# Kernel optimization log

Measured on AMD Instinct MI355X. Metric: run time of the kernel, lower is better.

## Reference

```python
import jax, jax.numpy as jnp
import numpy as np

EMBED_DIM = 1024
NUM_HEADS = 16
HEAD_DIM = EMBED_DIM // NUM_HEADS


def setup_inputs() -> dict:
    key = jax.random.key(0)
    ks = jax.random.split(key, 6)
    s = 1.0 / np.sqrt(EMBED_DIM)
    x = jax.random.normal(ks[0], (2, 2048, EMBED_DIM), dtype=jnp.float32)
    Wk = jax.random.uniform(ks[1], (EMBED_DIM, EMBED_DIM), jnp.float32, -s, s)
    Wq = jax.random.uniform(ks[2], (EMBED_DIM, EMBED_DIM), jnp.float32, -s, s)
    Wv = jax.random.uniform(ks[3], (EMBED_DIM, EMBED_DIM), jnp.float32, -s, s)
    Wo = jax.random.uniform(ks[4], (EMBED_DIM, EMBED_DIM), jnp.float32, -s, s)
    bo = jax.random.uniform(ks[5], (EMBED_DIM,), jnp.float32, -s, s)
    return {"x": x, "Wq": Wq, "Wk": Wk, "Wv": Wv, "Wo": Wo, "bo": bo}


def reference(x, Wq, Wk, Wv, Wo, bo):
    b, s, e = x.shape
    h, d = NUM_HEADS, HEAD_DIM
    scale = d ** (-0.5)
    # nn.Linear: y = x @ W.T ; here W stored as [out, in] -> use W.T
    q = (x @ Wq.T).reshape(b, s, h, d).transpose(0, 2, 1, 3)  # b h s d
    k = (x @ Wk.T).reshape(b, s, h, d).transpose(0, 2, 1, 3)
    v = (x @ Wv.T).reshape(b, s, h, d).transpose(0, 2, 1, 3)
    logits = jnp.einsum('bhqd,bhkd->bhqk', q, k) * scale
    attn = jax.nn.softmax(logits, axis=-1)
    out = jnp.einsum('bhqk,bhkd->bhqd', attn, v)
    out = out.transpose(0, 2, 1, 3).reshape(b, s, e)
    return out @ Wo.T + bo
```

## Files before the change

kernel.cpp:

```cpp
#include <hip/hip_runtime.h>
#include <hip/hip_bf16.h>

using short8 = __attribute__((ext_vector_type(8))) short;
using f32x4  = __attribute__((ext_vector_type(4))) float;
using uint4v = __attribute__((ext_vector_type(4))) unsigned;

#if __has_builtin(__builtin_amdgcn_exp2f)
#define EXP2(x) __builtin_amdgcn_exp2f(x)
#else
#define EXP2(x) exp2f(x)
#endif

#define SOFT_BARRIER()                                            \
    do {                                                          \
        asm volatile("s_waitcnt lgkmcnt(0)" ::: "memory");        \
        __builtin_amdgcn_s_barrier();                             \
    } while (0)

#define VM_BARRIER()                                              \
    do {                                                          \
        asm volatile("s_waitcnt vmcnt(0)" ::: "memory");          \
        __builtin_amdgcn_s_barrier();                             \
    } while (0)

__device__ __forceinline__ short f2bf(float f) {
    union { float f; unsigned u; } v; v.f = f;
    unsigned r = v.u + 0x7fffu + ((v.u >> 16) & 1u);
    return (short)(r >> 16);
}
__device__ __forceinline__ unsigned pack_trunc(float a, float b) {
    union { float f; unsigned u; } ua, ub; ua.f = a; ub.f = b;
#if __has_builtin(__builtin_amdgcn_perm)
    return __builtin_amdgcn_perm(ub.u, ua.u, 0x07060302u);
#else
    return (ub.u & 0xFFFF0000u) | (ua.u >> 16);
#endif
}
__device__ __forceinline__ void async_copy16(const short* g, short* s) {
    __builtin_amdgcn_global_load_lds(
        (const __attribute__((address_space(1))) void*)g,
        (__attribute__((address_space(3))) void*)s, 16, 0, 0);
}

__global__ __launch_bounds__(256) void cvt_f32_bf16(
    const float* __restrict__ s0, const float* __restrict__ s1,
    const float* __restrict__ s2, const float* __restrict__ s3,
    const float* __restrict__ s4,
    short* __restrict__ d0, short* __restrict__ d1, short* __restrict__ d2,
    short* __restrict__ d3, short* __restrict__ d4) {
    const int bid = blockIdx.x;
    const float* s; short* d; int base;
    if (bid < 4096) {
        s = s0; d = d0; base = bid << 10;
    } else {
        const int r = bid - 4096;
        base = (r & 1023) << 10;
        switch (r >> 10) {
            case 0: s = s1; d = d1; break;
            case 1: s = s2; d = d2; break;
            case 2: s = s3; d = d3; break;
            default: s = s4; d = d4; break;
        }
    }
    const int idx = base + threadIdx.x * 4;
    float4 v = *(const float4*)(s + idx);
    short4 o;
    o.x = f2bf(v.x); o.y = f2bf(v.y); o.z = f2bf(v.z); o.w = f2bf(v.w);
    *(short4*)(d + idx) = o;
}

template <int MODE>
__device__ __forceinline__ void gemm_body(const short* __restrict__ A,
                                          const short* __restrict__ B,
                                          short* __restrict__ C,
                                          float scale,
                                          short* __restrict__ As,
                                          short* __restrict__ Bs,
                                          int bm, int bn) {
    constexpr int Kd = 1024, Nd = 1024, Sd = 2048;
    constexpr int BUF = 128 * 64;

    const int tid  = threadIdx.x;
    const int w    = tid >> 6, lane = tid & 63;
    const int quad = lane >> 4, l16 = lane & 15;
    const int xr   = l16 & 7;
    const int wm   = (w >> 1) * 64, wn = (w & 1) * 64;

    f32x4 acc[4][4];
#pragma unroll
    for (int i = 0; i < 4; ++i)
#pragma unroll
        for (int j = 0; j < 4; ++j) acc[i][j] = (f32x4){0.f, 0.f, 0.f, 0.f};

    int lofs[4];
    const short *aga[4], *bga[4];
#pragma unroll
    for (int c = 0; c < 4; ++c) {
        const int li = c * 256 + tid, row = li >> 3;
        const int gcol = ((li & 7) ^ (row & 7)) * 8;
        lofs[c] = li * 8;
        aga[c]  = A + (size_t)(bm + row) * Kd + gcol;
        bga[c]  = B + (size_t)(bn + row) * Kd + gcol;
    }

    auto stage = [&](int k0, short* Ad, short* Bd) {
#pragma unroll
        for (int c = 0; c < 4; ++c) {
            async_copy16(aga[c] + k0, &Ad[lofs[c]]);
            async_copy16(bga[c] + k0, &Bd[lofs[c]]);
        }
    };

    auto compute = [&](const short* Ac, const short* Bc) {
#pragma unroll
        for (int kk = 0; kk < 2; ++kk) {
            short8 af[4], bfv[4];
#pragma unroll
            for (int mi = 0; mi < 4; ++mi) {
                const int r = wm + mi * 16 + l16;
                af[mi] = *(const short8*)(
                    &Ac[r * 64 + (((kk * 4 + quad) ^ xr) * 8)]);
            }
#pragma unroll
            for (int ni = 0; ni < 4; ++ni) {
                const int r = wn + ni * 16 + l16;
                bfv[ni] = *(const short8*)(
                    &Bc[r * 64 + (((kk * 4 + quad) ^ xr) * 8)]);
            }
#pragma unroll
            for (int mi = 0; mi < 4; ++mi)
#pragma unroll
                for (int ni = 0; ni < 4; ++ni) {
                    if constexpr (MODE == 2)
                        acc[mi][ni] = __builtin_amdgcn_mfma_f32_16x16x32_bf16(
                            bfv[ni], af[mi], acc[mi][ni], 0, 0, 0);
                    else
                        acc[mi][ni] = __builtin_amdgcn_mfma_f32_16x16x32_bf16(
                            af[mi], bfv[ni], acc[mi][ni], 0, 0, 0);
                }
        }
    };

    stage(0, As, Bs);
    VM_BARRIER();

#pragma unroll 1
    for (int ks = 0; ks < 16; ++ks) {
        if (ks + 1 < 16)
            stage((ks + 1) * 64, As + ((ks + 1) & 1) * BUF,
                  Bs + ((ks + 1) & 1) * BUF);
        compute(As + (ks & 1) * BUF, Bs + (ks & 1) * BUF);
        VM_BARRIER();
    }

    if constexpr (MODE == 2) {
#pragma unroll
        for (int mi = 0; mi < 4; ++mi) {
            const int m_g = bm + wm + mi * 16 + l16;
            const int b_  = m_g >> 11, s_ = m_g & 2047;
#pragma unroll
            for (int ni = 0; ni < 4; ++ni)
#pragma unroll
                for (int r = 0; r < 4; ++r) {
                    const int n_g = bn + wn + ni * 16 + quad * 4 + r;
                    C[(size_t)b_ * Nd * Sd + (size_t)n_g * Sd + s_] =
                        f2bf(acc[mi][ni][r]);
                }
        }
    } else {
#pragma unroll
        for (int ni = 0; ni < 4; ++ni) {
            const int colg = bn + wn + ni * 16 + l16;
#pragma unroll
            for (int mi = 0; mi < 4; ++mi)
#pragma unroll
                for (int r = 0; r < 4; ++r) {
                    const int rowg = bm + wm + mi * 16 + quad * 4 + r;
                    C[(size_t)rowg * Nd + colg] = f2bf(acc[mi][ni][r] * scale);
                }
        }
    }
}

#define CSC 0.18033688f

__global__ __launch_bounds__(256, 2) void proj_gemm(
    const short* __restrict__ X,
    const short* __restrict__ Wq, const short* __restrict__ Wk,
    const short* __restrict__ Wv,
    short* __restrict__ Qo, short* __restrict__ Ko, short* __restrict__ VTo) {
    __shared__ __align__(16) short As[2 * 128 * 64];
    __shared__ __align__(16) short Bs[2 * 128 * 64];

    const int bid = blockIdx.x;
    const int xcd = bid & 7, idx = bid >> 3;
    const int z   = idx >> 5;
    const int rem = idx & 31;
    const int bm  = (((xcd >> 1) * 8) + (rem >> 2)) * 128;
    const int bn  = (((xcd & 1) * 4) + (rem & 3)) * 128;

    if (z == 0)
        gemm_body<0>(X, Wq, Qo, CSC, As, Bs, bm, bn);
    else if (z == 1)
        gemm_body<0>(X, Wk, Ko, 1.0f, As, Bs, bm, bn);
    else
        gemm_body<2>(X, Wv, VTo, 1.0f, As, Bs, bm, bn);
}

__global__ __launch_bounds__(256, 2) void out_gemm(
    const short* __restrict__ A, const short* __restrict__ B,
    const float* __restrict__ bias, float* __restrict__ C) {
    constexpr int Kd = 1024, Nd = 1024;
    constexpr int ABUF = 64 * 64, BBUF = 128 * 64;
    __shared__ __align__(16) short As[2 * ABUF];
    __shared__ __align__(16) short Bs[2 * BBUF];

    const int tid  = threadIdx.x;
    const int w    = tid >> 6, lane = tid & 63;
    const int quad = lane >> 4, l16 = lane & 15;
    const int xr   = l16 & 7;
    const int wm   = (w >> 1) * 32, wn = (w & 1) * 64;

    const int bid = blockIdx.x;
    const int xcd = bid & 7, idx = bid >> 3;
    const int bm  = (((xcd >> 1) * 16) + (idx >> 2)) * 64;
    const int bn  = (((xcd & 1) * 4) + (idx & 3)) * 128;

    f32x4 acc[2][4];
#pragma unroll
    for (int i = 0; i < 2; ++i)
#pragma unroll
        for (int j = 0; j < 4; ++j) acc[i][j] = (f32x4){0.f, 0.f, 0.f, 0.f};

    int aofs[2], bofs[4];
    const short *aga[2], *bga[4];
#pragma unroll
    for (int c = 0; c < 2; ++c) {
        const int li = c * 256 + tid, row = li >> 3;
        const int gcol = ((li & 7) ^ (row & 7)) * 8;
        aofs[c] = li * 8;
        aga[c]  = A + (size_t)(bm + row) * Kd + gcol;
    }
#pragma unroll
    for (int c = 0; c < 4; ++c) {
        const int li = c * 256 + tid, row = li >> 3;
        const int gcol = ((li & 7) ^ (row & 7)) * 8;
        bofs[c] = li * 8;
        bga[c]  = B + (size_t)(bn + row) * Kd + gcol;
    }

    auto stage = [&](int k0, short* Ad, short* Bd) {
#pragma unroll
        for (int c = 0; c < 2; ++c) async_copy16(aga[c] + k0, &Ad[aofs[c]]);
#pragma unroll
        for (int c = 0; c < 4; ++c) async_copy16(bga[c] + k0, &Bd[bofs[c]]);
    };

    auto compute = [&](const short* Ac, const short* Bc) {
#pragma unroll
        for (int kk = 0; kk < 2; ++kk) {
            short8 af[2], bfv[4];
#pragma unroll
            for (int mi = 0; mi < 2; ++mi) {
                const int r = wm + mi * 16 + l16;
                af[mi] = *(const short8*)(
                    &Ac[r * 64 + (((kk * 4 + quad) ^ xr) * 8)]);
            }
#pragma unroll
            for (int ni = 0; ni < 4; ++ni) {
                const int r = wn + ni * 16 + l16;
                bfv[ni] = *(const short8*)(
                    &Bc[r * 64 + (((kk * 4 + quad) ^ xr) * 8)]);
            }
#pragma unroll
            for (int mi = 0; mi < 2; ++mi)
#pragma unroll
                for (int ni = 0; ni < 4; ++ni)
                    acc[mi][ni] = __builtin_amdgcn_mfma_f32_16x16x32_bf16(
                        af[mi], bfv[ni], acc[mi][ni], 0, 0, 0);
        }
    };

    stage(0, As, Bs);
    VM_BARRIER();

#pragma unroll 1
    for (int ks = 0; ks < 16; ++ks) {
        if (ks + 1 < 16)
            stage((ks + 1) * 64, As + ((ks + 1) & 1) * ABUF,
                  Bs + ((ks + 1) & 1) * BBUF);
        compute(As + (ks & 1) * ABUF, Bs + (ks & 1) * BBUF);
        VM_BARRIER();
    }

#pragma unroll
    for (int ni = 0; ni < 4; ++ni) {
        const int colg = bn + wn + ni * 16 + l16;
        const float bv = bias[colg];
#pragma unroll
        for (int mi = 0; mi < 2; ++mi)
#pragma unroll
            for (int r = 0; r < 4; ++r) {
                const int rowg = bm + wm + mi * 16 + quad * 4 + r;
                C[(size_t)rowg * Nd + colg] = acc[mi][ni][r] + bv;
            }
    }
}

__global__ __launch_bounds__(256, 2) void attn_kernel(
    const short* __restrict__ Q, const short* __restrict__ K,
    const short* __restrict__ VT, short* __restrict__ O) {
    constexpr int S = 2048, E = 1024, NT = S / 64;
    __shared__ __align__(16) short Ks[2][64 * 64];
    __shared__ __align__(16) short Vs[3][64 * 64];

    const int tid  = threadIdx.x;
    const int w    = tid >> 6, lane = tid & 63;
    const int quad = lane >> 4, l16 = lane & 15;

    const int bid  = blockIdx.x;
    const int xcd  = bid & 7, slot = bid >> 3;
    const int qt   = slot & 15;
    const int bh   = xcd + ((slot >> 4) << 3);
    const int b    = bh >> 4, h = bh & 15;

    const int    q0   = qt * 128 + w * 32;
    const size_t base = (size_t)b * S * E;
    const size_t vtb  = (size_t)b * E * S;
    const int    hc   = h * 64;
    const int    xr   = l16 & 7;

    short8 aq[2][2];
#pragma unroll
    for (int qg = 0; qg < 2; ++qg) {
        const short* qp = Q + base + (size_t)(q0 + qg * 16 + l16) * E + hc + quad * 8;
        aq[qg][0] = *(const short8*)(qp);
        aq[qg][1] = *(const short8*)(qp + 32);
    }

    f32x4 oT[2][4], o_sum[2];
#pragma unroll
    for (int qg = 0; qg < 2; ++qg) {
        o_sum[qg] = (f32x4){0.f, 0.f, 0.f, 0.f};
#pragma unroll
        for (int i = 0; i < 4; ++i) oT[qg][i] = (f32x4){0.f, 0.f, 0.f, 0.f};
    }

    int          kdst[2], vdst0[2], vdst1[2];
    const short* kga[2];
    const short* vga[2];
#pragma unroll
    for (int c = 0; c < 2; ++c) {
        int li = c * 256 + tid, row = li >> 3, cc = li & 7;
        kdst[c] = row * 64 + ((cc ^ (row & 7)) * 8);
        int c0   = 4 * (cc >> 2) + 2 * (cc & 1);
        int boff = 4 * ((cc >> 1) & 1);
        vdst0[c] = row * 64 + ((c0 ^ (row & 7)) * 8) + boff;
        vdst1[c] = row * 64 + (((c0 + 1) ^ (row & 7)) * 8) + boff;
        kga[c]   = K + base + (size_t)row * E + hc + cc * 8;
        vga[c]   = VT + vtb + (size_t)(hc + row) * S + cc * 8;
    }

    short8 kr[2], vr[2];
    auto load_regs = [&](int t) {
#pragma unroll
        for (int c = 0; c < 2; ++c) {
            kr[c] = *(const short8*)(kga[c] + (size_t)t * 64 * E);
            vr[c] = *(const short8*)(vga[c] + t * 64);
        }
    };
    auto store_regs = [&](short* Kn, short* Vn) {
#pragma unroll
        for (int c = 0; c < 2; ++c) {
            *(short8*)(&Kn[kdst[c]]) = kr[c];
            short4 lo, hi;
            lo.x = vr[c][0]; lo.y = vr[c][1]; lo.z = vr[c][2]; lo.w = vr[c][3];
            hi.x = vr[c][4]; hi.y = vr[c][5]; hi.z = vr[c][6]; hi.w = vr[c][7];
            *(short4*)(&Vn[vdst0[c]]) = lo;
            *(short4*)(&Vn[vdst1[c]]) = hi;
        }
    };

    const short8 ones = (short8){0x3F80, 0x3F80, 0x3F80, 0x3F80,
                                 0x3F80, 0x3F80, 0x3F80, 0x3F80};
    const float  LB   = 0.00281502f;

    uint4v pkvA[2][2], pkvB[2][2];

    auto qk_half = [&](const short* Kc, uint4v (&pc)[2][2], int h) {
#pragma unroll
        for (int kh = 0; kh < 2; ++kh) {
            const int    kn  = h * 2 + kh;
            const short* kb  = &Kc[(kn * 16 + l16) * 64];
            short8       bk0 = *(const short8*)(kb + ((quad ^ xr) * 8));
            short8       bk1 = *(const short8*)(kb + (((quad + 4) ^ xr) * 8));
#pragma unroll
            for (int qg = 0; qg < 2; ++qg) {
                f32x4 a = (f32x4){LB, LB, LB, LB};
                a = __builtin_amdgcn_mfma_f32_16x16x32_bf16(bk0, aq[qg][0], a, 0, 0, 0);
                a = __builtin_amdgcn_mfma_f32_16x16x32_bf16(bk1, aq[qg][1], a, 0, 0, 0);
                pc[qg][h][kh * 2]     = pack_trunc(EXP2(a[0]), EXP2(a[1]));
                pc[qg][h][kh * 2 + 1] = pack_trunc(EXP2(a[2]), EXP2(a[3]));
            }
        }
    };
    auto pv_half = [&](const short* Vp, uint4v (&pp)[2][2], int ks) {
        short8 pf[2];
#pragma unroll
        for (int qg = 0; qg < 2; ++qg) {
            union { uint4v u; short8 s; } cv;
            cv.u   = pp[qg][ks];
            pf[qg] = cv.s;
            o_sum[qg] = __builtin_amdgcn_mfma_f32_16x16x32_bf16(
                ones, pf[qg], o_sum[qg], 0, 0, 0);
        }
#pragma unroll
        for (int ni = 0; ni < 4; ++ni) {
            const int rv = ni * 16 + l16;
            short8 vb =
                *(const short8*)(&Vp[rv * 64 + (((ks * 4 + quad) ^ xr) * 8)]);
#pragma unroll
            for (int qg = 0; qg < 2; ++qg)
                oT[qg][ni] = __builtin_amdgcn_mfma_f32_16x16x32_bf16(
                    vb, pf[qg], oT[qg][ni], 0, 0, 0);
        }
    };

    auto body = [&](int kt, uint4v (&pp)[2][2], uint4v (&pc)[2][2]) {
        if (kt + 1 < NT) {
            store_regs(Ks[(kt + 1) & 1], Vs[(kt + 1) % 3]);
            if (kt + 2 < NT) load_regs(kt + 2);
        }
        const short* Kc = Ks[kt & 1];
        const short* Vp = Vs[(kt - 1) % 3];
        __builtin_amdgcn_s_setprio(1);
        pv_half(Vp, pp, 0);
        qk_half(Kc, pc, 0);
        pv_half(Vp, pp, 1);
        qk_half(Kc, pc, 1);
        __builtin_amdgcn_s_setprio(0);
        SOFT_BARRIER();
    };

    load_regs(0);
    store_regs(Ks[0], Vs[0]);
    load_regs(1);
    SOFT_BARRIER();
    store_regs(Ks[1], Vs[1]);
    load_regs(2);
    __builtin_amdgcn_s_setprio(1);
    qk_half(Ks[0], pkvA, 0);
    qk_half(Ks[0], pkvA, 1);
    __builtin_amdgcn_s_setprio(0);
    SOFT_BARRIER();

#pragma unroll 1
    for (int kt = 1; kt < NT - 1; kt += 2) {
        body(kt, pkvA, pkvB);
        body(kt + 1, pkvB, pkvA);
    }
    body(NT - 1, pkvA, pkvB);
    __builtin_amdgcn_s_setprio(1);
    pv_half(Vs[(NT - 1) % 3], pkvB, 0);
    pv_half(Vs[(NT - 1) % 3], pkvB, 1);
    __builtin_amdgcn_s_setprio(0);

#pragma unroll
    for (int qg = 0; qg < 2; ++qg) {
        const float inv = 1.0f / o_sum[qg][0];
        const int   qg_ = q0 + qg * 16 + l16;
#pragma unroll
        for (int ni = 0; ni < 4; ++ni) {
            short4 ov;
            ov.x = f2bf(oT[qg][ni][0] * inv);
            ov.y = f2bf(oT[qg][ni][1] * inv);
            ov.z = f2bf(oT[qg][ni][2] * inv);
            ov.w = f2bf(oT[qg][ni][3] * inv);
            *(short4*)(&O[base + (size_t)qg_ * E + hc + ni * 16 + quad * 4]) = ov;
        }
    }
}

extern "C" void kernel_launch(void* const* d_in, const int* in_sizes, int n_in,
                              void* d_out, int out_size, void* d_ws, size_t ws_size,
                              hipStream_t stream) {
    const float* x  = (const float*)d_in[0];
    const float* Wq = (const float*)d_in[1];
    const float* Wk = (const float*)d_in[2];
    const float* Wv = (const float*)d_in[3];
    const float* Wo = (const float*)d_in[4];
    const float* bo = (const float*)d_in[5];
    float* out = (float*)d_out;

    constexpr int XN = 2 * 2048 * 1024;
    constexpr int WN = 1024 * 1024;

    short* Xb  = (short*)d_ws;
    short* Wqb = Xb + XN;
    short* Wkb = Wqb + WN;
    short* Wvb = Wkb + WN;
    short* Wob = Wvb + WN;
    short* Qb  = Wob + WN;
    short* Kb  = Qb + XN;
    short* VTb = Kb + XN;

    cvt_f32_bf16<<<dim3(8192), 256, 0, stream>>>(
        x, Wq, Wk, Wv, Wo, Xb, Wqb, Wkb, Wvb, Wob);
    proj_gemm<<<dim3(768), 256, 0, stream>>>(Xb, Wqb, Wkb, Wvb, Qb, Kb, VTb);
    attn_kernel<<<dim3(512), 256, 0, stream>>>(Qb, Kb, VTb, Xb );
    out_gemm<<<dim3(512), 256, 0, stream>>>(Xb, Wob, bo, out);
}
```

Before: 172.7 us.

## Replace double-buffered projection GEMM pipeline with single buffer and higher occupancy

```diff
diff --git a/kernel.cpp b/kernel.cpp
--- a/kernel.cpp
+++ b/kernel.cpp
@@ -78,7 +78,6 @@
                                           short* __restrict__ Bs,
                                           int bm, int bn) {
     constexpr int Kd = 1024, Nd = 1024, Sd = 2048;
-    constexpr int BUF = 128 * 64;
 
     const int tid  = threadIdx.x;
     const int w    = tid >> 6, lane = tid & 63;
@@ -92,26 +91,18 @@
 #pragma unroll
         for (int j = 0; j < 4; ++j) acc[i][j] = (f32x4){0.f, 0.f, 0.f, 0.f};
 
-    int lofs[4];
-    const short *aga[4], *bga[4];
-#pragma unroll
-    for (int c = 0; c < 4; ++c) {
-        const int li = c * 256 + tid, row = li >> 3;
-        const int gcol = ((li & 7) ^ (row & 7)) * 8;
-        lofs[c] = li * 8;
-        aga[c]  = A + (size_t)(bm + row) * Kd + gcol;
-        bga[c]  = B + (size_t)(bn + row) * Kd + gcol;
-    }
-
-    auto stage = [&](int k0, short* Ad, short* Bd) {
+    for (int k0 = 0; k0 < Kd; k0 += 64) {
+        __syncthreads();
 #pragma unroll
         for (int c = 0; c < 4; ++c) {
-            async_copy16(aga[c] + k0, &Ad[lofs[c]]);
-            async_copy16(bga[c] + k0, &Bd[lofs[c]]);
-        }
-    };
-
-    auto compute = [&](const short* Ac, const short* Bc) {
+            int li   = c * 256 + tid;
+            int row  = li >> 3;
+            int gcol = ((li & 7) ^ (row & 7)) * 8;
+            async_copy16(A + (size_t)(bm + row) * Kd + k0 + gcol, &As[li * 8]);
+            async_copy16(B + (size_t)(bn + row) * Kd + k0 + gcol, &Bs[li * 8]);
+        }
+        __syncthreads();
+
 #pragma unroll
         for (int kk = 0; kk < 2; ++kk) {
             short8 af[4], bfv[4];
@@ -119,13 +110,13 @@
             for (int mi = 0; mi < 4; ++mi) {
                 const int r = wm + mi * 16 + l16;
                 af[mi] = *(const short8*)(
-                    &Ac[r * 64 + (((kk * 4 + quad) ^ xr) * 8)]);
+                    &As[r * 64 + (((kk * 4 + quad) ^ xr) * 8)]);
             }
 #pragma unroll
             for (int ni = 0; ni < 4; ++ni) {
                 const int r = wn + ni * 16 + l16;
                 bfv[ni] = *(const short8*)(
-                    &Bc[r * 64 + (((kk * 4 + quad) ^ xr) * 8)]);
+                    &Bs[r * 64 + (((kk * 4 + quad) ^ xr) * 8)]);
             }
 #pragma unroll
             for (int mi = 0; mi < 4; ++mi)
@@ -139,18 +130,6 @@
                             af[mi], bfv[ni], acc[mi][ni], 0, 0, 0);
                 }
         }
-    };
-
-    stage(0, As, Bs);
-    VM_BARRIER();
-
-#pragma unroll 1
-    for (int ks = 0; ks < 16; ++ks) {
-        if (ks + 1 < 16)
-            stage((ks + 1) * 64, As + ((ks + 1) & 1) * BUF,
-                  Bs + ((ks + 1) & 1) * BUF);
-        compute(As + (ks & 1) * BUF, Bs + (ks & 1) * BUF);
-        VM_BARRIER();
     }
 
     if constexpr (MODE == 2) {
@@ -184,13 +163,13 @@
 
 #define CSC 0.18033688f
 
-__global__ __launch_bounds__(256, 2) void proj_gemm(
+__global__ __launch_bounds__(256, 3) void proj_gemm(
     const short* __restrict__ X,
     const short* __restrict__ Wq, const short* __restrict__ Wk,
     const short* __restrict__ Wv,
     short* __restrict__ Qo, short* __restrict__ Ko, short* __restrict__ VTo) {
-    __shared__ __align__(16) short As[2 * 128 * 64];
-    __shared__ __align__(16) short Bs[2 * 128 * 64];
+    __shared__ __align__(16) short As[128 * 64];
+    __shared__ __align__(16) short Bs[128 * 64];
 
     const int bid = blockIdx.x;
     const int xcd = bid & 7, idx = bid >> 3;
```

Result: faster. 165.6 us (-4.1%).
